# Performance work log

Hardware: AMD Instinct MI355X
Metric: run time of the kernel (lower is better)

Reference implementation:

```python
import jax, jax.numpy as jnp
import numpy as np

N_NODES = 100000
N_EDGES = 1600000
F_IN, H1, H2, N_CLS = 512, 180, 120, 40
NEG_SLOPE = 0.01  # F.leaky_relu default


def setup_inputs() -> dict:
    key = jax.random.key(0)
    ks = jax.random.split(key, 8)
    x = jax.random.normal(ks[0], (N_NODES, F_IN), dtype=jnp.float32)
    edge_index = jax.random.randint(ks[1], (2, N_EDGES), 0, N_NODES, dtype=jnp.int64)
    W1 = jax.random.normal(ks[2], (F_IN, H1), dtype=jnp.float32) / np.sqrt(F_IN)
    b1 = jnp.zeros((H1,), dtype=jnp.float32)
    W2 = jax.random.normal(ks[3], (H1, H2), dtype=jnp.float32) / np.sqrt(H1)
    b2 = jnp.zeros((H2,), dtype=jnp.float32)
    W3 = jax.random.normal(ks[4], (H2, N_CLS), dtype=jnp.float32) / np.sqrt(H2)
    b3 = jnp.zeros((N_CLS,), dtype=jnp.float32)
    return {"x": x, "edge_index": edge_index, "W1": W1, "b1": b1,
            "W2": W2, "b2": b2, "W3": W3, "b3": b3}


def _add_self_loops(edge_index, n):
    loop = jnp.arange(n, dtype=edge_index.dtype)
    src = jnp.concatenate([edge_index[0], loop])
    dst = jnp.concatenate([edge_index[1], loop])
    return src, dst


def _gcn_conv(h, src, dst, norm, W, b, n):
    # PyG GCNConv: linear transform first, then normalized scatter-add at dst.
    h = h @ W  # [N, out]
    msg = norm[:, None] * h[src]  # gather at source, per-edge scale
    out = jax.ops.segment_sum(msg, dst, num_segments=n)  # scatter-add at dest
    return out + b


def reference(x, edge_index, W1, b1, W2, b2, W3, b3):
    n = x.shape[0]
    src, dst = _add_self_loops(edge_index, n)
    # symmetric normalization deg^-1/2 * deg^-1/2 on self-loop-augmented graph
    ones = jnp.ones(dst.shape[0], dtype=x.dtype)
    deg = jax.ops.segment_sum(ones, dst, num_segments=n)
    dinv = jnp.where(deg > 0, jax.lax.rsqrt(deg), 0.0)
    norm = dinv[src] * dinv[dst]  # [E+N]

    h = _gcn_conv(x, src, dst, norm, W1, b1, n)
    h = jnp.where(h >= 0, h, NEG_SLOPE * h)
    h = _gcn_conv(h, src, dst, norm, W2, b2, n)
    h = jnp.where(h >= 0, h, NEG_SLOPE * h)
    logits = h @ W3 + b3
    return jax.nn.log_softmax(logits, axis=1)
```

## Files before the change

### kernel.cpp

```cpp
#include <hip/hip_runtime.h>
#include <math.h>

typedef __attribute__((ext_vector_type(8))) short short8;
typedef __attribute__((ext_vector_type(4))) float f32x4;

static constexpr int F_IN = 512;
static constexpr int H1V = 180, H1P = 192;
static constexpr int H2V = 120, H2P = 128;
static constexpr int NC  = 40,  NCP = 64;

__device__ inline unsigned f2bf(float f) {
    unsigned u = __float_as_uint(f);
    return (u + 0x7fffu + ((u >> 16) & 1u)) >> 16;
}
__device__ inline unsigned cvtpk(float lo, float hi) {
    unsigned r;
    asm("v_cvt_pk_bf16_f32 %0, %1, %2" : "=v"(r) : "v"(lo), "v"(hi));
    return r;
}
#define BLO(u) __uint_as_float((u) << 16)
#define BHI(u) __uint_as_float((u) & 0xffff0000u)

__device__ inline void gload_lds16(const void* gsrc, void* ldst) {
    __builtin_amdgcn_global_load_lds(
        (const __attribute__((address_space(1))) void*)gsrc,
        (__attribute__((address_space(3))) void*)ldst, 16, 0, 0);
}

__global__ void k_detect(const int* __restrict__ ei, int* __restrict__ flag) {
    int i = blockIdx.x * 256 + threadIdx.x;
    if (ei[2 * i + 1] != 0) flag[0] = 0;
}

__global__ void k_hist(const int* __restrict__ ei, int E, const int* __restrict__ flag,
                       int* __restrict__ deg, int* __restrict__ rank) {
    int e = blockIdx.x * 256 + threadIdx.x;
    if (e >= E) return;
    int d = flag[0] ? ei[2 * E + 2 * e] : ei[E + e];
    rank[e] = atomicAdd(&deg[d], 1);
}

__global__ void k_scan1(const int* __restrict__ deg, int* __restrict__ rp,
                        int* __restrict__ bsum, float* __restrict__ dinv, int n) {
    __shared__ int s[256];
    int t = threadIdx.x;
    int base = blockIdx.x * 1024 + t * 4;
    int v0 = (base + 0 < n) ? deg[base + 0] : 0;
    int v1 = (base + 1 < n) ? deg[base + 1] : 0;
    int v2 = (base + 2 < n) ? deg[base + 2] : 0;
    int v3 = (base + 3 < n) ? deg[base + 3] : 0;
    if (base + 0 < n) dinv[base + 0] = rsqrtf((float)(v0 + 1));
    if (base + 1 < n) dinv[base + 1] = rsqrtf((float)(v1 + 1));
    if (base + 2 < n) dinv[base + 2] = rsqrtf((float)(v2 + 1));
    if (base + 3 < n) dinv[base + 3] = rsqrtf((float)(v3 + 1));
    int sum = v0 + v1 + v2 + v3;
    s[t] = sum;
    __syncthreads();
    for (int off = 1; off < 256; off <<= 1) {
        int x = (t >= off) ? s[t - off] : 0;
        __syncthreads();
        s[t] += x;
        __syncthreads();
    }
    int run = s[t] - sum;
    if (t == 255) bsum[blockIdx.x] = s[255];
    if (base + 0 < n) rp[base + 0] = run; run += v0;
    if (base + 1 < n) rp[base + 1] = run; run += v1;
    if (base + 2 < n) rp[base + 2] = run; run += v2;
    if (base + 3 < n) rp[base + 3] = run;
}

__global__ void k_scan2(int* __restrict__ bsum, int nb) {
    __shared__ int s[128];
    int t = threadIdx.x;
    int v = (t < nb) ? bsum[t] : 0;
    s[t] = v;
    __syncthreads();
    for (int off = 1; off < 128; off <<= 1) {
        int x = (t >= off) ? s[t - off] : 0;
        __syncthreads();
        s[t] += x;
        __syncthreads();
    }
    if (t < nb) bsum[t] = s[t] - v;
}

__global__ void k_scan3(const int* __restrict__ bsum, int* __restrict__ rp,
                        int n, int E) {
    int i = blockIdx.x * 256 + threadIdx.x;
    if (i < n) {
        rp[i] = rp[i] + bsum[i >> 10];
    } else if (i == n) {
        rp[n] = E;
    }
}

__global__ __launch_bounds__(256) void k_fill(const int* __restrict__ ei, int E,
                                              const int* __restrict__ flag,
                                              const int* __restrict__ rp,
                                              const int* __restrict__ rank,
                                              int* __restrict__ csr,
                                              int bw, int chunk) {
    int bkt = blockIdx.x & 7;
    int lo = bkt * bw, hi = lo + bw;
    int ch = blockIdx.x >> 3;
    int e0 = ch * chunk;
    int e1 = min(E, e0 + chunk);
    bool i64 = flag[0] != 0;
    for (int e = e0 + (int)threadIdx.x; e < e1; e += 256) {
        int d = i64 ? ei[2 * E + 2 * e] : ei[E + e];
        if (d >= lo && d < hi) {
            int s = i64 ? ei[2 * e] : ei[e];
            csr[rp[d] + rank[e]] = s;
        }
    }
}

__global__ void k_prep(const float* __restrict__ W1, const float* __restrict__ W2,
                       const float* __restrict__ W3, const float* __restrict__ b1,
                       const float* __restrict__ b2, const float* __restrict__ b3,
                       unsigned short* __restrict__ W1s, unsigned short* __restrict__ W2s,
                       unsigned short* __restrict__ W3s, float* __restrict__ b1p,
                       float* __restrict__ b2p, float* __restrict__ b3p) {
    const int n1 = F_IN * H1P;
    const int n2 = n1 + H1P * H2P;
    const int n3 = n2 + H2P * NCP;
    const int n4 = n3 + H1P;
    const int n5 = n4 + H2P;
    const int n6 = n5 + NCP;
    int i = blockIdx.x * 256 + threadIdx.x;
    if (i < n1) {
        int k = i / H1P, c = i % H1P;
        float v = (c < H1V) ? W1[k * H1V + c] : 0.0f;
        W1s[(size_t)(k >> 3) * H1P * 8 + c * 8 + (k & 7)] = (unsigned short)f2bf(v);
    } else if (i < n2) {
        int j = i - n1;
        int k = j / H2P, c = j % H2P;
        float v = (k < H1V && c < H2V) ? W2[k * H2V + c] : 0.0f;
        W2s[(size_t)(k >> 3) * H2P * 8 + c * 8 + (k & 7)] = (unsigned short)f2bf(v);
    } else if (i < n3) {
        int j = i - n2;
        int k = j / NCP, c = j % NCP;
        float v = (k < H2V && c < NC) ? W3[k * NC + c] : 0.0f;
        W3s[(size_t)(k >> 3) * NCP * 8 + c * 8 + (k & 7)] = (unsigned short)f2bf(v);
    } else if (i < n4) {
        int c = i - n3;
        b1p[c] = (c < H1V) ? b1[c] : 0.0f;
    } else if (i < n5) {
        int c = i - n4;
        b2p[c] = (c < H2V) ? b2[c] : 0.0f;
    } else if (i < n6) {
        int c = i - n5;
        b3p[c] = (c < NC) ? b3[c] : -1e30f;
    }
}

__global__ __launch_bounds__(512) void k_gemm1(const float* __restrict__ X,
                                               const short8* __restrict__ Bs,
                                               const float* __restrict__ dinv,
                                               unsigned short* __restrict__ Hout,
                                               int M) {
    __shared__ float ldsf[8192];
    char* lds = (char*)ldsf;
    int t = threadIdx.x;
    int w = t >> 6, l = t & 63;
    int lr = l & 15, kg = l >> 4;
    int wr = w >> 2, wc = w & 3;
    int row0 = blockIdx.x * 128;
    int colb = wc * 48;

    f32x4 acc[4][3];
#pragma unroll
    for (int m = 0; m < 4; ++m)
#pragma unroll
        for (int nn = 0; nn < 3; ++nn) acc[m][nn] = (f32x4){0.f, 0.f, 0.f, 0.f};

    auto stage = [&](int kb, int buf) {
#pragma unroll
        for (int j = 0; j < 2; ++j) {
            int o = j * 8192 + t * 16;
            int row = o >> 7;
            int col4 = ((o >> 4) & 7) ^ (row & 7);
            int rowg = row0 + row;
            if (rowg >= M) rowg = M - 1;
            gload_lds16(X + (size_t)rowg * F_IN + kb + col4 * 4,
                        lds + buf * 16384 + j * 8192 + w * 1024);
        }
    };

    stage(0, 0);
    __syncthreads();

    for (int ts = 0; ts < 16; ++ts) {
        int cur = ts & 1;
        if (ts < 15) stage((ts + 1) * 32, cur ^ 1);
        short8 b[3];
#pragma unroll
        for (int nn = 0; nn < 3; ++nn)
            b[nn] = Bs[(size_t)(ts * 4 + kg) * H1P + colb + nn * 16 + lr];
        short8 a[4];
#pragma unroll
        for (int m = 0; m < 4; ++m) {
            int row = wr * 64 + m * 16 + lr;
            char* base = lds + cur * 16384 + row * 128;
            float4 v0 = *(const float4*)(base + (((2 * kg + 0) ^ (row & 7)) * 16));
            float4 v1 = *(const float4*)(base + (((2 * kg + 1) ^ (row & 7)) * 16));
            union { unsigned u[4]; short8 s; } cu;
            cu.u[0] = cvtpk(v0.x, v0.y);
            cu.u[1] = cvtpk(v0.z, v0.w);
            cu.u[2] = cvtpk(v1.x, v1.y);
            cu.u[3] = cvtpk(v1.z, v1.w);
            a[m] = cu.s;
        }
#pragma unroll
        for (int m = 0; m < 4; ++m)
#pragma unroll
            for (int nn = 0; nn < 3; ++nn)
                acc[m][nn] = __builtin_amdgcn_mfma_f32_16x16x32_bf16(a[m], b[nn], acc[m][nn], 0, 0, 0);
        __syncthreads();
    }

#pragma unroll
    for (int m = 0; m < 4; ++m) {
        int r4 = row0 + wr * 64 + m * 16 + kg * 4;
#pragma unroll
        for (int j = 0; j < 4; ++j) {
            int grow = r4 + j;
            if (grow < M) {
                float dv = dinv[grow];
#pragma unroll
                for (int nn = 0; nn < 3; ++nn)
                    Hout[(size_t)grow * H1P + colb + nn * 16 + lr] =
                        (unsigned short)f2bf(acc[m][nn][j] * dv);
            }
        }
    }
}

__global__ __launch_bounds__(512) void k_gemm2(const unsigned short* __restrict__ A,
                                               const short8* __restrict__ Bs,
                                               const float* __restrict__ dinv,
                                               unsigned short* __restrict__ Hout,
                                               int M) {
    __shared__ unsigned short ldsu[16384];
    char* lds = (char*)ldsu;
    int t = threadIdx.x;
    int w = t >> 6, l = t & 63;
    int lr = l & 15, kg = l >> 4;
    int wr = w >> 2, wc = w & 3;
    int row0 = blockIdx.x * 128;
    int colb = wc * 32;

    f32x4 acc[4][2];
#pragma unroll
    for (int m = 0; m < 4; ++m)
#pragma unroll
        for (int nn = 0; nn < 2; ++nn) acc[m][nn] = (f32x4){0.f, 0.f, 0.f, 0.f};

    auto stage = [&](int kb, int buf) {
#pragma unroll
        for (int j = 0; j < 2; ++j) {
            int o = j * 8192 + t * 16;
            int row = o >> 7;
            int chunk = ((o >> 4) & 7) ^ (row & 7);
            int rowg = row0 + row;
            if (rowg >= M) rowg = M - 1;
            gload_lds16(A + (size_t)rowg * H1P + kb + chunk * 8,
                        lds + buf * 16384 + j * 8192 + w * 1024);
        }
    };

    stage(0, 0);
    __syncthreads();

    for (int ts = 0; ts < 3; ++ts) {
        int cur = ts & 1;
        if (ts < 2) stage((ts + 1) * 64, cur ^ 1);
        short8 b[2][2];
#pragma unroll
        for (int kk = 0; kk < 2; ++kk)
#pragma unroll
            for (int nn = 0; nn < 2; ++nn)
                b[kk][nn] = Bs[(size_t)(ts * 8 + kk * 4 + kg) * H2P + colb + nn * 16 + lr];
        short8 a[2][4];
#pragma unroll
        for (int kk = 0; kk < 2; ++kk)
#pragma unroll
            for (int m = 0; m < 4; ++m) {
                int row = wr * 64 + m * 16 + lr;
                a[kk][m] = *(const short8*)(lds + cur * 16384 + row * 128 +
                                            (((kk * 4 + kg) ^ (row & 7)) * 16));
            }
#pragma unroll
        for (int kk = 0; kk < 2; ++kk)
#pragma unroll
            for (int m = 0; m < 4; ++m)
#pragma unroll
                for (int nn = 0; nn < 2; ++nn)
                    acc[m][nn] = __builtin_amdgcn_mfma_f32_16x16x32_bf16(a[kk][m], b[kk][nn], acc[m][nn], 0, 0, 0);
        __syncthreads();
    }

#pragma unroll
    for (int m = 0; m < 4; ++m) {
        int r4 = row0 + wr * 64 + m * 16 + kg * 4;
#pragma unroll
        for (int j = 0; j < 4; ++j) {
            int grow = r4 + j;
            if (grow < M) {
                float dv = dinv[grow];
#pragma unroll
                for (int nn = 0; nn < 2; ++nn)
                    Hout[(size_t)grow * H2P + colb + nn * 16 + lr] =
                        (unsigned short)f2bf(acc[m][nn][j] * dv);
            }
        }
    }
}

template <int CH, int OUTBF>
__global__ __launch_bounds__(256) void k_gat(const uint2* __restrict__ H,
                                             const float* __restrict__ dinv,
                                             const int* __restrict__ rp,
                                             const int* __restrict__ csr,
                                             const float* __restrict__ bias,
                                             void* __restrict__ outv, int n) {
    int wv = threadIdx.x >> 6, l = threadIdx.x & 63;
    int i = blockIdx.x * 4 + wv;
    if (i >= n) return;
    bool act = l < CH;
    int c = act ? l : 0;
    const uint2* Hr = H + c;

    float a0, a1, a2, a3;
    {
        uint2 v = Hr[(size_t)i * CH];
        a0 = BLO(v.x); a1 = BHI(v.x); a2 = BLO(v.y); a3 = BHI(v.y);
    }
    float p0 = 0.f, p1 = 0.f, p2 = 0.f, p3 = 0.f;

    int e0 = rp[i], e1 = rp[i + 1];
    int e = e0;
    for (; e + 7 < e1; e += 8) {
        int s[8];
#pragma unroll
        for (int q = 0; q < 8; ++q) s[q] = csr[e + q];
        uint2 v[8];
#pragma unroll
        for (int q = 0; q < 8; ++q) v[q] = Hr[(size_t)s[q] * CH];
#pragma unroll
        for (int q = 0; q < 8; q += 2) {
            a0 += BLO(v[q].x); a1 += BHI(v[q].x); a2 += BLO(v[q].y); a3 += BHI(v[q].y);
            p0 += BLO(v[q + 1].x); p1 += BHI(v[q + 1].x); p2 += BLO(v[q + 1].y); p3 += BHI(v[q + 1].y);
        }
    }
    for (; e + 3 < e1; e += 4) {
        int s0 = csr[e], s1 = csr[e + 1], s2 = csr[e + 2], s3 = csr[e + 3];
        uint2 va = Hr[(size_t)s0 * CH];
        uint2 vb = Hr[(size_t)s1 * CH];
        uint2 vc = Hr[(size_t)s2 * CH];
        uint2 vd = Hr[(size_t)s3 * CH];
        a0 += BLO(va.x); a1 += BHI(va.x); a2 += BLO(va.y); a3 += BHI(va.y);
        p0 += BLO(vb.x); p1 += BHI(vb.x); p2 += BLO(vb.y); p3 += BHI(vb.y);
        a0 += BLO(vc.x); a1 += BHI(vc.x); a2 += BLO(vc.y); a3 += BHI(vc.y);
        p0 += BLO(vd.x); p1 += BHI(vd.x); p2 += BLO(vd.y); p3 += BHI(vd.y);
    }
    for (; e < e1; ++e) {
        int s0 = csr[e];
        uint2 va = Hr[(size_t)s0 * CH];
        a0 += BLO(va.x); a1 += BHI(va.x); a2 += BLO(va.y); a3 += BHI(va.y);
    }
    a0 += p0; a1 += p1; a2 += p2; a3 += p3;

    float di = dinv[i];
    float4 bb = *(const float4*)(bias + 4 * c);
    float o0 = fmaf(di, a0, bb.x);
    float o1 = fmaf(di, a1, bb.y);
    float o2 = fmaf(di, a2, bb.z);
    float o3 = fmaf(di, a3, bb.w);
    o0 = o0 >= 0.f ? o0 : 0.01f * o0;
    o1 = o1 >= 0.f ? o1 : 0.01f * o1;
    o2 = o2 >= 0.f ? o2 : 0.01f * o2;
    o3 = o3 >= 0.f ? o3 : 0.01f * o3;
    if (act) {
        if (OUTBF) {
            uint2 r;
            r.x = (f2bf(o1) << 16) | f2bf(o0);
            r.y = (f2bf(o3) << 16) | f2bf(o2);
            ((uint2*)outv)[(size_t)i * CH + c] = r;
        } else {
            ((float4*)outv)[(size_t)i * CH + c] = make_float4(o0, o1, o2, o3);
        }
    }
}

__global__ __launch_bounds__(256) void k_gat2(const uint2* __restrict__ H,
                                              const float* __restrict__ dinv,
                                              const int* __restrict__ rp,
                                              const int* __restrict__ csr,
                                              const float* __restrict__ bias,
                                              uint2* __restrict__ out, int n) {
    int wv = threadIdx.x >> 6, l = threadIdx.x & 63;
    int half = l >> 5, c = l & 31;
    int i = blockIdx.x * 8 + wv * 2 + half;
    if (i >= n) return;
    const uint2* Hr = H + c;

    float a0, a1, a2, a3;
    {
        uint2 v = Hr[(size_t)i * 32];
        a0 = BLO(v.x); a1 = BHI(v.x); a2 = BLO(v.y); a3 = BHI(v.y);
    }
    float p0 = 0.f, p1 = 0.f, p2 = 0.f, p3 = 0.f;

    int e0 = rp[i], e1 = rp[i + 1];
    int e = e0;
    for (; e + 7 < e1; e += 8) {
        int s[8];
#pragma unroll
        for (int q = 0; q < 8; ++q) s[q] = csr[e + q];
        uint2 v[8];
#pragma unroll
        for (int q = 0; q < 8; ++q) v[q] = Hr[(size_t)s[q] * 32];
#pragma unroll
        for (int q = 0; q < 8; q += 2) {
            a0 += BLO(v[q].x); a1 += BHI(v[q].x); a2 += BLO(v[q].y); a3 += BHI(v[q].y);
            p0 += BLO(v[q + 1].x); p1 += BHI(v[q + 1].x); p2 += BLO(v[q + 1].y); p3 += BHI(v[q + 1].y);
        }
    }
    for (; e + 3 < e1; e += 4) {
        int s0 = csr[e], s1 = csr[e + 1], s2 = csr[e + 2], s3 = csr[e + 3];
        uint2 va = Hr[(size_t)s0 * 32];
        uint2 vb = Hr[(size_t)s1 * 32];
        uint2 vc = Hr[(size_t)s2 * 32];
        uint2 vd = Hr[(size_t)s3 * 32];
        a0 += BLO(va.x); a1 += BHI(va.x); a2 += BLO(va.y); a3 += BHI(va.y);
        p0 += BLO(vb.x); p1 += BHI(vb.x); p2 += BLO(vb.y); p3 += BHI(vb.y);
        a0 += BLO(vc.x); a1 += BHI(vc.x); a2 += BLO(vc.y); a3 += BHI(vc.y);
        p0 += BLO(vd.x); p1 += BHI(vd.x); p2 += BLO(vd.y); p3 += BHI(vd.y);
    }
    for (; e < e1; ++e) {
        int s0 = csr[e];
        uint2 va = Hr[(size_t)s0 * 32];
        a0 += BLO(va.x); a1 += BHI(va.x); a2 += BLO(va.y); a3 += BHI(va.y);
    }
    a0 += p0; a1 += p1; a2 += p2; a3 += p3;

    float di = dinv[i];
    float4 bb = *(const float4*)(bias + 4 * c);
    float o0 = fmaf(di, a0, bb.x);
    float o1 = fmaf(di, a1, bb.y);
    float o2 = fmaf(di, a2, bb.z);
    float o3 = fmaf(di, a3, bb.w);
    o0 = o0 >= 0.f ? o0 : 0.01f * o0;
    o1 = o1 >= 0.f ? o1 : 0.01f * o1;
    o2 = o2 >= 0.f ? o2 : 0.01f * o2;
    o3 = o3 >= 0.f ? o3 : 0.01f * o3;
    uint2 r;
    r.x = (f2bf(o1) << 16) | f2bf(o0);
    r.y = (f2bf(o3) << 16) | f2bf(o2);
    out[(size_t)i * 32 + c] = r;
}

__global__ __launch_bounds__(256) void k_out(const unsigned short* __restrict__ H,
                                             const short8* __restrict__ Bs,
                                             const float* __restrict__ b3p,
                                             float* __restrict__ out, int M) {
    int t = threadIdx.x;
    int w = t >> 6, l = t & 63;
    int lr = l & 15, kg = l >> 4;
    int row0 = blockIdx.x * 64 + w * 16;

    f32x4 acc[4];
#pragma unroll
    for (int f = 0; f < 4; ++f) acc[f] = (f32x4){0.f, 0.f, 0.f, 0.f};

    int rowa = row0 + lr;
    if (rowa >= M) rowa = M - 1;
    const unsigned short* arow = H + (size_t)rowa * H2P;

#pragma unroll
    for (int ks = 0; ks < 4; ++ks) {
        short8 a = *(const short8*)(arow + ks * 32 + kg * 8);
#pragma unroll
        for (int f = 0; f < 4; ++f) {
            short8 b = Bs[(size_t)(ks * 4 + kg) * NCP + f * 16 + lr];
            acc[f] = __builtin_amdgcn_mfma_f32_16x16x32_bf16(a, b, acc[f], 0, 0, 0);
        }
    }

    float bl[4];
#pragma unroll
    for (int f = 0; f < 4; ++f) bl[f] = b3p[f * 16 + lr];

#pragma unroll
    for (int j = 0; j < 4; ++j) {
        int grow = row0 + kg * 4 + j;
        float lg[4];
#pragma unroll
        for (int f = 0; f < 4; ++f) lg[f] = acc[f][j] + bl[f];
        float m = fmaxf(fmaxf(lg[0], lg[1]), fmaxf(lg[2], lg[3]));
#pragma unroll
        for (int d = 1; d < 16; d <<= 1) m = fmaxf(m, __shfl_xor(m, d));
        float s = expf(lg[0] - m) + expf(lg[1] - m) + expf(lg[2] - m) + expf(lg[3] - m);
#pragma unroll
        for (int d = 1; d < 16; d <<= 1) s += __shfl_xor(s, d);
        float lse = m + logf(s);
        if (grow < M) {
#pragma unroll
            for (int f = 0; f < 4; ++f) {
                int c = f * 16 + lr;
                if (c < NC) out[(size_t)grow * NC + c] = lg[f] - lse;
            }
        }
    }
}

extern "C" void kernel_launch(void* const* d_in, const int* in_sizes, int n_in,
                              void* d_out, int out_size, void* d_ws, size_t ws_size,
                              hipStream_t stream) {
    const float* x  = (const float*)d_in[0];
    const int*   ei = (const int*)d_in[1];
    const float* W1 = (const float*)d_in[2];
    const float* b1 = (const float*)d_in[3];
    const float* W2 = (const float*)d_in[4];
    const float* b2 = (const float*)d_in[5];
    const float* W3 = (const float*)d_in[6];
    const float* b3 = (const float*)d_in[7];
    float* outp = (float*)d_out;

    int n = in_sizes[0] / F_IN;
    int E = in_sizes[1] / 2;

    char* p = (char*)d_ws;
    auto alloc = [&](size_t bytes) -> char* {
        char* r = p;
        p += (bytes + 511) & ~(size_t)511;
        return r;
    };
    int*            flag   = (int*)alloc(4);
    int*            deg    = (int*)alloc((size_t)n * 4);
    float*          dinv   = (float*)alloc((size_t)n * 4);
    int*            rp     = (int*)alloc((size_t)(n + 1) * 4);
    int*            bsum   = (int*)alloc(4096);
    int*            rank   = (int*)alloc((size_t)E * 4);
    int*            csr    = (int*)alloc((size_t)E * 4);
    unsigned short* W1s    = (unsigned short*)alloc((size_t)F_IN * H1P * 2);
    unsigned short* W2s    = (unsigned short*)alloc((size_t)H1P * H2P * 2);
    unsigned short* W3s    = (unsigned short*)alloc((size_t)H2P * NCP * 2);
    float*          b1p    = (float*)alloc(H1P * 4);
    float*          b2p    = (float*)alloc(H2P * 4);
    float*          b3p    = (float*)alloc(NCP * 4);
    unsigned short* h1     = (unsigned short*)alloc((size_t)n * H1P * 2);
    unsigned short* h1agg  = (unsigned short*)alloc((size_t)n * H1P * 2);
    unsigned short* h2     = (unsigned short*)alloc((size_t)n * H2P * 2);
    unsigned short* h2agg  = (unsigned short*)alloc((size_t)n * H2P * 2);

    hipMemsetAsync(flag, 1, 4, stream);
    hipMemsetAsync(deg, 0, (size_t)n * 4, stream);

    k_detect<<<16, 256, 0, stream>>>(ei, flag);

    int eb = (E + 255) / 256;
    k_hist<<<eb, 256, 0, stream>>>(ei, E, flag, deg, rank);

    int nb = (n + 1023) / 1024;
    k_scan1<<<nb, 256, 0, stream>>>(deg, rp, bsum, dinv, n);
    k_scan2<<<1, 128, 0, stream>>>(bsum, nb);
    k_scan3<<<(n + 1 + 255) / 256, 256, 0, stream>>>(bsum, rp, n, E);

    int bw = (n + 7) / 8;
    int nch = 256;
    int chunk = (E + nch - 1) / nch;
    k_fill<<<nch * 8, 256, 0, stream>>>(ei, E, flag, rp, rank, csr, bw, chunk);

    k_prep<<<514, 256, 0, stream>>>(W1, W2, W3, b1, b2, b3, W1s, W2s, W3s, b1p, b2p, b3p);

    int gb = (n + 127) / 128;
    k_gemm1<<<gb, 512, 0, stream>>>(x, (const short8*)W1s, dinv, h1, n);
    k_gat<H1P / 4, 1><<<(n + 3) / 4, 256, 0, stream>>>((const uint2*)h1, dinv, rp, csr, b1p, h1agg, n);
    k_gemm2<<<gb, 512, 0, stream>>>(h1agg, (const short8*)W2s, dinv, h2, n);
    k_gat2<<<(n + 7) / 8, 256, 0, stream>>>((const uint2*)h2, dinv, rp, csr, b2p, (uint2*)h2agg, n);
    k_out<<<(n + 63) / 64, 256, 0, stream>>>(h2agg, (const short8*)W3s, b3p, outp, n);
}
```

Baseline: 377.6 us.

## Quantize layer-1 features to int8 with per-row scales for aggregation

The first GEMM now emits int8 features with a per-row scale, computed by a cross-wave row-max reduction through LDS, instead of bf16. A new gather kernel dequantizes while accumulating neighbours, so each per-edge gather reads 4 bytes per lane instead of 8, halving the traffic of the first aggregation. Separately, weight prep and index-width detection are merged into one init kernel and the flag and degree memsets into one, removing a launch and a memset. The int8 step adds quantization error on top of bf16 and an extra scale load per edge.

```diff
diff --git a/kernel.cpp b/kernel.cpp
--- a/kernel.cpp
+++ b/kernel.cpp
@@ -27,108 +27,25 @@
         (__attribute__((address_space(3))) void*)ldst, 16, 0, 0);
 }
 
-__global__ void k_detect(const int* __restrict__ ei, int* __restrict__ flag) {
-    int i = blockIdx.x * 256 + threadIdx.x;
-    if (ei[2 * i + 1] != 0) flag[0] = 0;
-}
-
-__global__ void k_hist(const int* __restrict__ ei, int E, const int* __restrict__ flag,
-                       int* __restrict__ deg, int* __restrict__ rank) {
-    int e = blockIdx.x * 256 + threadIdx.x;
-    if (e >= E) return;
-    int d = flag[0] ? ei[2 * E + 2 * e] : ei[E + e];
-    rank[e] = atomicAdd(&deg[d], 1);
-}
-
-__global__ void k_scan1(const int* __restrict__ deg, int* __restrict__ rp,
-                        int* __restrict__ bsum, float* __restrict__ dinv, int n) {
-    __shared__ int s[256];
-    int t = threadIdx.x;
-    int base = blockIdx.x * 1024 + t * 4;
-    int v0 = (base + 0 < n) ? deg[base + 0] : 0;
-    int v1 = (base + 1 < n) ? deg[base + 1] : 0;
-    int v2 = (base + 2 < n) ? deg[base + 2] : 0;
-    int v3 = (base + 3 < n) ? deg[base + 3] : 0;
-    if (base + 0 < n) dinv[base + 0] = rsqrtf((float)(v0 + 1));
-    if (base + 1 < n) dinv[base + 1] = rsqrtf((float)(v1 + 1));
-    if (base + 2 < n) dinv[base + 2] = rsqrtf((float)(v2 + 1));
-    if (base + 3 < n) dinv[base + 3] = rsqrtf((float)(v3 + 1));
-    int sum = v0 + v1 + v2 + v3;
-    s[t] = sum;
-    __syncthreads();
-    for (int off = 1; off < 256; off <<= 1) {
-        int x = (t >= off) ? s[t - off] : 0;
-        __syncthreads();
-        s[t] += x;
-        __syncthreads();
-    }
-    int run = s[t] - sum;
-    if (t == 255) bsum[blockIdx.x] = s[255];
-    if (base + 0 < n) rp[base + 0] = run; run += v0;
-    if (base + 1 < n) rp[base + 1] = run; run += v1;
-    if (base + 2 < n) rp[base + 2] = run; run += v2;
-    if (base + 3 < n) rp[base + 3] = run;
-}
-
-__global__ void k_scan2(int* __restrict__ bsum, int nb) {
-    __shared__ int s[128];
-    int t = threadIdx.x;
-    int v = (t < nb) ? bsum[t] : 0;
-    s[t] = v;
-    __syncthreads();
-    for (int off = 1; off < 128; off <<= 1) {
-        int x = (t >= off) ? s[t - off] : 0;
-        __syncthreads();
-        s[t] += x;
-        __syncthreads();
-    }
-    if (t < nb) bsum[t] = s[t] - v;
-}
-
-__global__ void k_scan3(const int* __restrict__ bsum, int* __restrict__ rp,
-                        int n, int E) {
-    int i = blockIdx.x * 256 + threadIdx.x;
-    if (i < n) {
-        rp[i] = rp[i] + bsum[i >> 10];
-    } else if (i == n) {
-        rp[n] = E;
-    }
-}
-
-__global__ __launch_bounds__(256) void k_fill(const int* __restrict__ ei, int E,
-                                              const int* __restrict__ flag,
-                                              const int* __restrict__ rp,
-                                              const int* __restrict__ rank,
-                                              int* __restrict__ csr,
-                                              int bw, int chunk) {
-    int bkt = blockIdx.x & 7;
-    int lo = bkt * bw, hi = lo + bw;
-    int ch = blockIdx.x >> 3;
-    int e0 = ch * chunk;
-    int e1 = min(E, e0 + chunk);
-    bool i64 = flag[0] != 0;
-    for (int e = e0 + (int)threadIdx.x; e < e1; e += 256) {
-        int d = i64 ? ei[2 * E + 2 * e] : ei[E + e];
-        if (d >= lo && d < hi) {
-            int s = i64 ? ei[2 * e] : ei[e];
-            csr[rp[d] + rank[e]] = s;
-        }
-    }
-}
-
-__global__ void k_prep(const float* __restrict__ W1, const float* __restrict__ W2,
+__global__ void k_init(const int* __restrict__ ei, int* __restrict__ flag,
+                       const float* __restrict__ W1, const float* __restrict__ W2,
                        const float* __restrict__ W3, const float* __restrict__ b1,
                        const float* __restrict__ b2, const float* __restrict__ b3,
                        unsigned short* __restrict__ W1s, unsigned short* __restrict__ W2s,
                        unsigned short* __restrict__ W3s, float* __restrict__ b1p,
                        float* __restrict__ b2p, float* __restrict__ b3p) {
+    if (blockIdx.x < 16) {
+        int i = blockIdx.x * 256 + threadIdx.x;
+        if (ei[2 * i + 1] != 0) flag[0] = 1;
+        return;
+    }
     const int n1 = F_IN * H1P;
     const int n2 = n1 + H1P * H2P;
     const int n3 = n2 + H2P * NCP;
     const int n4 = n3 + H1P;
     const int n5 = n4 + H2P;
     const int n6 = n5 + NCP;
-    int i = blockIdx.x * 256 + threadIdx.x;
+    int i = (blockIdx.x - 16) * 256 + threadIdx.x;
     if (i < n1) {
         int k = i / H1P, c = i % H1P;
         float v = (c < H1V) ? W1[k * H1V + c] : 0.0f;
@@ -155,10 +72,96 @@
     }
 }
 
+__global__ void k_hist(const int* __restrict__ ei, int E, const int* __restrict__ flag,
+                       int* __restrict__ deg, int* __restrict__ rank) {
+    int e = blockIdx.x * 256 + threadIdx.x;
+    if (e >= E) return;
+    bool i64 = (flag[0] == 0);
+    int d = i64 ? ei[2 * E + 2 * e] : ei[E + e];
+    rank[e] = atomicAdd(&deg[d], 1);
+}
+
+__global__ void k_scan1(const int* __restrict__ deg, int* __restrict__ rp,
+                        int* __restrict__ bsum, float* __restrict__ dinv, int n) {
+    __shared__ int s[256];
+    int t = threadIdx.x;
+    int base = blockIdx.x * 1024 + t * 4;
+    int v0 = (base + 0 < n) ? deg[base + 0] : 0;
+    int v1 = (base + 1 < n) ? deg[base + 1] : 0;
+    int v2 = (base + 2 < n) ? deg[base + 2] : 0;
+    int v3 = (base + 3 < n) ? deg[base + 3] : 0;
+    if (base + 0 < n) dinv[base + 0] = rsqrtf((float)(v0 + 1));
+    if (base + 1 < n) dinv[base + 1] = rsqrtf((float)(v1 + 1));
+    if (base + 2 < n) dinv[base + 2] = rsqrtf((float)(v2 + 1));
+    if (base + 3 < n) dinv[base + 3] = rsqrtf((float)(v3 + 1));
+    int sum = v0 + v1 + v2 + v3;
+    s[t] = sum;
+    __syncthreads();
+    for (int off = 1; off < 256; off <<= 1) {
+        int x = (t >= off) ? s[t - off] : 0;
+        __syncthreads();
+        s[t] += x;
+        __syncthreads();
+    }
+    int run = s[t] - sum;
+    if (t == 255) bsum[blockIdx.x] = s[255];
+    if (base + 0 < n) rp[base + 0] = run; run += v0;
+    if (base + 1 < n) rp[base + 1] = run; run += v1;
+    if (base + 2 < n) rp[base + 2] = run; run += v2;
+    if (base + 3 < n) rp[base + 3] = run;
+}
+
+__global__ void k_scan2(int* __restrict__ bsum, int nb) {
+    __shared__ int s[128];
+    int t = threadIdx.x;
+    int v = (t < nb) ? bsum[t] : 0;
+    s[t] = v;
+    __syncthreads();
+    for (int off = 1; off < 128; off <<= 1) {
+        int x = (t >= off) ? s[t - off] : 0;
+        __syncthreads();
+        s[t] += x;
+        __syncthreads();
+    }
+    if (t < nb) bsum[t] = s[t] - v;
+}
+
+__global__ void k_scan3(const int* __restrict__ bsum, int* __restrict__ rp,
+                        int n, int E) {
+    int i = blockIdx.x * 256 + threadIdx.x;
+    if (i < n) {
+        rp[i] = rp[i] + bsum[i >> 10];
+    } else if (i == n) {
+        rp[n] = E;
+    }
+}
+
+__global__ __launch_bounds__(256) void k_fill(const int* __restrict__ ei, int E,
+                                              const int* __restrict__ flag,
+                                              const int* __restrict__ rp,
+                                              const int* __restrict__ rank,
+                                              int* __restrict__ csr,
+                                              int bw, int chunk) {
+    int bkt = blockIdx.x & 7;
+    int lo = bkt * bw, hi = lo + bw;
+    int ch = blockIdx.x >> 3;
+    int e0 = ch * chunk;
+    int e1 = min(E, e0 + chunk);
+    bool i64 = (flag[0] == 0);
+    for (int e = e0 + (int)threadIdx.x; e < e1; e += 256) {
+        int d = i64 ? ei[2 * E + 2 * e] : ei[E + e];
+        if (d >= lo && d < hi) {
+            int s = i64 ? ei[2 * e] : ei[e];
+            csr[rp[d] + rank[e]] = s;
+        }
+    }
+}
+
 __global__ __launch_bounds__(512) void k_gemm1(const float* __restrict__ X,
                                                const short8* __restrict__ Bs,
                                                const float* __restrict__ dinv,
-                                               unsigned short* __restrict__ Hout,
+                                               signed char* __restrict__ Hq,
+                                               float* __restrict__ sc,
                                                int M) {
     __shared__ float ldsf[8192];
     char* lds = (char*)ldsf;
@@ -220,20 +223,122 @@
         __syncthreads();
     }
 
+    float* rmaxp = (float*)lds;
 #pragma unroll
     for (int m = 0; m < 4; ++m) {
-        int r4 = row0 + wr * 64 + m * 16 + kg * 4;
 #pragma unroll
         for (int j = 0; j < 4; ++j) {
-            int grow = r4 + j;
-            if (grow < M) {
-                float dv = dinv[grow];
-#pragma unroll
-                for (int nn = 0; nn < 3; ++nn)
-                    Hout[(size_t)grow * H1P + colb + nn * 16 + lr] =
-                        (unsigned short)f2bf(acc[m][nn][j] * dv);
+            int rl = wr * 64 + m * 16 + kg * 4 + j;
+            int grow = row0 + rl;
+            float dv = (grow < M) ? dinv[grow] : 0.f;
+            float lm = 0.f;
+#pragma unroll
+            for (int nn = 0; nn < 3; ++nn)
+                lm = fmaxf(lm, fabsf(acc[m][nn][j] * dv));
+#pragma unroll
+            for (int d = 1; d < 16; d <<= 1)
+                lm = fmaxf(lm, __shfl_xor(lm, d));
+            if (lr == 0) rmaxp[rl * 4 + wc] = lm;
+        }
+    }
+    __syncthreads();
+#pragma unroll
+    for (int m = 0; m < 4; ++m) {
+#pragma unroll
+        for (int j = 0; j < 4; ++j) {
+            int rl = wr * 64 + m * 16 + kg * 4 + j;
+            int grow = row0 + rl;
+            if (grow >= M) continue;
+            float dv = dinv[grow];
+            float rm = fmaxf(fmaxf(rmaxp[rl * 4 + 0], rmaxp[rl * 4 + 1]),
+                             fmaxf(rmaxp[rl * 4 + 2], rmaxp[rl * 4 + 3]));
+            float inv = (rm > 0.f) ? 127.0f / rm : 0.f;
+            if (wc == 0 && lr == 0) sc[grow] = rm * (1.0f / 127.0f);
+#pragma unroll
+            for (int nn = 0; nn < 3; ++nn) {
+                float v = acc[m][nn][j] * dv * inv;
+                v = fminf(fmaxf(rintf(v), -127.f), 127.f);
+                Hq[(size_t)grow * H1P + colb + nn * 16 + lr] = (signed char)(int)v;
             }
         }
+    }
+}
+
+__global__ __launch_bounds__(256) void k_gat1q(const signed char* __restrict__ Hq,
+                                               const float* __restrict__ sc,
+                                               const float* __restrict__ dinv,
+                                               const int* __restrict__ rp,
+                                               const int* __restrict__ csr,
+                                               const float* __restrict__ bias,
+                                               uint2* __restrict__ out, int n) {
+    int wv = threadIdx.x >> 6, l = threadIdx.x & 63;
+    int i = blockIdx.x * 4 + wv;
+    if (i >= n) return;
+    bool act = l < 48;
+    int c = act ? l : 0;
+    const unsigned* Hr = (const unsigned*)(Hq + c * 4);
+
+    float a0, a1, a2, a3;
+    {
+        unsigned w0 = Hr[(size_t)i * 48];
+        float s0 = sc[i];
+        a0 = (float)(signed char)(w0) * s0;
+        a1 = (float)(signed char)(w0 >> 8) * s0;
+        a2 = (float)(signed char)(w0 >> 16) * s0;
+        a3 = (float)(signed char)(w0 >> 24) * s0;
+    }
+    float p0 = 0.f, p1 = 0.f, p2 = 0.f, p3 = 0.f;
+
+    int e0 = rp[i], e1 = rp[i + 1];
+    int e = e0;
+    for (; e + 7 < e1; e += 8) {
+        int s[8];
+#pragma unroll
+        for (int q = 0; q < 8; ++q) s[q] = csr[e + q];
+        float scs[8];
+#pragma unroll
+        for (int q = 0; q < 8; ++q) scs[q] = sc[s[q]];
+        unsigned v[8];
+#pragma unroll
+        for (int q = 0; q < 8; ++q) v[q] = Hr[(size_t)s[q] * 48];
+#pragma unroll
+        for (int q = 0; q < 8; q += 2) {
+            a0 = fmaf((float)(signed char)(v[q]), scs[q], a0);
+            a1 = fmaf((float)(signed char)(v[q] >> 8), scs[q], a1);
+            a2 = fmaf((float)(signed char)(v[q] >> 16), scs[q], a2);
+            a3 = fmaf((float)(signed char)(v[q] >> 24), scs[q], a3);
+            p0 = fmaf((float)(signed char)(v[q + 1]), scs[q + 1], p0);
+            p1 = fmaf((float)(signed char)(v[q + 1] >> 8), scs[q + 1], p1);
+            p2 = fmaf((float)(signed char)(v[q + 1] >> 16), scs[q + 1], p2);
+            p3 = fmaf((float)(signed char)(v[q + 1] >> 24), scs[q + 1], p3);
+        }
+    }
+    for (; e < e1; ++e) {
+        int s0 = csr[e];
+        float sq = sc[s0];
+        unsigned w0 = Hr[(size_t)s0 * 48];
+        a0 = fmaf((float)(signed char)(w0), sq, a0);
+        a1 = fmaf((float)(signed char)(w0 >> 8), sq, a1);
+        a2 = fmaf((float)(signed char)(w0 >> 16), sq, a2);
+        a3 = fmaf((float)(signed char)(w0 >> 24), sq, a3);
+    }
+    a0 += p0; a1 += p1; a2 += p2; a3 += p3;
+
+    float di = dinv[i];
+    float4 bb = *(const float4*)(bias + 4 * c);
+    float o0 = fmaf(di, a0, bb.x);
+    float o1 = fmaf(di, a1, bb.y);
+    float o2 = fmaf(di, a2, bb.z);
+    float o3 = fmaf(di, a3, bb.w);
+    o0 = o0 >= 0.f ? o0 : 0.01f * o0;
+    o1 = o1 >= 0.f ? o1 : 0.01f * o1;
+    o2 = o2 >= 0.f ? o2 : 0.01f * o2;
+    o3 = o3 >= 0.f ? o3 : 0.01f * o3;
+    if (act) {
+        uint2 r;
+        r.x = (f2bf(o1) << 16) | f2bf(o0);
+        r.y = (f2bf(o3) << 16) | f2bf(o2);
+        out[(size_t)i * 48 + c] = r;
     }
 }
 
@@ -314,82 +419,6 @@
                     Hout[(size_t)grow * H2P + colb + nn * 16 + lr] =
                         (unsigned short)f2bf(acc[m][nn][j] * dv);
             }
-        }
-    }
-}
-
-template <int CH, int OUTBF>
-__global__ __launch_bounds__(256) void k_gat(const uint2* __restrict__ H,
-                                             const float* __restrict__ dinv,
-                                             const int* __restrict__ rp,
-                                             const int* __restrict__ csr,
-                                             const float* __restrict__ bias,
-                                             void* __restrict__ outv, int n) {
-    int wv = threadIdx.x >> 6, l = threadIdx.x & 63;
-    int i = blockIdx.x * 4 + wv;
-    if (i >= n) return;
-    bool act = l < CH;
-    int c = act ? l : 0;
-    const uint2* Hr = H + c;
-
-    float a0, a1, a2, a3;
-    {
-        uint2 v = Hr[(size_t)i * CH];
-        a0 = BLO(v.x); a1 = BHI(v.x); a2 = BLO(v.y); a3 = BHI(v.y);
-    }
-    float p0 = 0.f, p1 = 0.f, p2 = 0.f, p3 = 0.f;
-
-    int e0 = rp[i], e1 = rp[i + 1];
-    int e = e0;
-    for (; e + 7 < e1; e += 8) {
-        int s[8];
-#pragma unroll
-        for (int q = 0; q < 8; ++q) s[q] = csr[e + q];
-        uint2 v[8];
-#pragma unroll
-        for (int q = 0; q < 8; ++q) v[q] = Hr[(size_t)s[q] * CH];
-#pragma unroll
-        for (int q = 0; q < 8; q += 2) {
-            a0 += BLO(v[q].x); a1 += BHI(v[q].x); a2 += BLO(v[q].y); a3 += BHI(v[q].y);
-            p0 += BLO(v[q + 1].x); p1 += BHI(v[q + 1].x); p2 += BLO(v[q + 1].y); p3 += BHI(v[q + 1].y);
-        }
-    }
-    for (; e + 3 < e1; e += 4) {
-        int s0 = csr[e], s1 = csr[e + 1], s2 = csr[e + 2], s3 = csr[e + 3];
-        uint2 va = Hr[(size_t)s0 * CH];
-        uint2 vb = Hr[(size_t)s1 * CH];
-        uint2 vc = Hr[(size_t)s2 * CH];
-        uint2 vd = Hr[(size_t)s3 * CH];
-        a0 += BLO(va.x); a1 += BHI(va.x); a2 += BLO(va.y); a3 += BHI(va.y);
-        p0 += BLO(vb.x); p1 += BHI(vb.x); p2 += BLO(vb.y); p3 += BHI(vb.y);
-        a0 += BLO(vc.x); a1 += BHI(vc.x); a2 += BLO(vc.y); a3 += BHI(vc.y);
-        p0 += BLO(vd.x); p1 += BHI(vd.x); p2 += BLO(vd.y); p3 += BHI(vd.y);
-    }
-    for (; e < e1; ++e) {
-        int s0 = csr[e];
-        uint2 va = Hr[(size_t)s0 * CH];
-        a0 += BLO(va.x); a1 += BHI(va.x); a2 += BLO(va.y); a3 += BHI(va.y);
-    }
-    a0 += p0; a1 += p1; a2 += p2; a3 += p3;
-
-    float di = dinv[i];
-    float4 bb = *(const float4*)(bias + 4 * c);
-    float o0 = fmaf(di, a0, bb.x);
-    float o1 = fmaf(di, a1, bb.y);
-    float o2 = fmaf(di, a2, bb.z);
-    float o3 = fmaf(di, a3, bb.w);
-    o0 = o0 >= 0.f ? o0 : 0.01f * o0;
-    o1 = o1 >= 0.f ? o1 : 0.01f * o1;
-    o2 = o2 >= 0.f ? o2 : 0.01f * o2;
-    o3 = o3 >= 0.f ? o3 : 0.01f * o3;
-    if (act) {
-        if (OUTBF) {
-            uint2 r;
-            r.x = (f2bf(o1) << 16) | f2bf(o0);
-            r.y = (f2bf(o3) << 16) | f2bf(o2);
-            ((uint2*)outv)[(size_t)i * CH + c] = r;
-        } else {
-            ((float4*)outv)[(size_t)i * CH + c] = make_float4(o0, o1, o2, o3);
         }
     }
 }
@@ -538,8 +567,9 @@
         p += (bytes + 511) & ~(size_t)511;
         return r;
     };
-    int*            flag   = (int*)alloc(4);
-    int*            deg    = (int*)alloc((size_t)n * 4);
+    int*            fd     = (int*)alloc((size_t)(n + 1) * 4);
+    int*            flag   = fd;
+    int*            deg    = fd + 1;
     float*          dinv   = (float*)alloc((size_t)n * 4);
     int*            rp     = (int*)alloc((size_t)(n + 1) * 4);
     int*            bsum   = (int*)alloc(4096);
@@ -551,15 +581,16 @@
     float*          b1p    = (float*)alloc(H1P * 4);
     float*          b2p    = (float*)alloc(H2P * 4);
     float*          b3p    = (float*)alloc(NCP * 4);
-    unsigned short* h1     = (unsigned short*)alloc((size_t)n * H1P * 2);
+    signed char*    h1q    = (signed char*)alloc((size_t)n * H1P);
+    float*          sc     = (float*)alloc((size_t)n * 4);
     unsigned short* h1agg  = (unsigned short*)alloc((size_t)n * H1P * 2);
     unsigned short* h2     = (unsigned short*)alloc((size_t)n * H2P * 2);
     unsigned short* h2agg  = (unsigned short*)alloc((size_t)n * H2P * 2);
 
-    hipMemsetAsync(flag, 1, 4, stream);
-    hipMemsetAsync(deg, 0, (size_t)n * 4, stream);
-
-    k_detect<<<16, 256, 0, stream>>>(ei, flag);
+    hipMemsetAsync(fd, 0, (size_t)(n + 1) * 4, stream);
+
+    k_init<<<530, 256, 0, stream>>>(ei, flag, W1, W2, W3, b1, b2, b3,
+                                    W1s, W2s, W3s, b1p, b2p, b3p);
 
     int eb = (E + 255) / 256;
     k_hist<<<eb, 256, 0, stream>>>(ei, E, flag, deg, rank);
@@ -574,12 +605,12 @@
     int chunk = (E + nch - 1) / nch;
     k_fill<<<nch * 8, 256, 0, stream>>>(ei, E, flag, rp, rank, csr, bw, chunk);
 
-    k_prep<<<514, 256, 0, stream>>>(W1, W2, W3, b1, b2, b3, W1s, W2s, W3s, b1p, b2p, b3p);
-
     int gb = (n + 127) / 128;
-    k_gemm1<<<gb, 512, 0, stream>>>(x, (const short8*)W1s, dinv, h1, n);
-    k_gat<H1P / 4, 1><<<(n + 3) / 4, 256, 0, stream>>>((const uint2*)h1, dinv, rp, csr, b1p, h1agg, n);
+    k_gemm1<<<gb, 512, 0, stream>>>(x, (const short8*)W1s, dinv, h1q, sc, n);
+    k_gat1q<<<(n + 3) / 4, 256, 0, stream>>>(h1q, sc, dinv, rp, csr, b1p,
+                                             (uint2*)h1agg, n);
     k_gemm2<<<gb, 512, 0, stream>>>(h1agg, (const short8*)W2s, dinv, h2, n);
-    k_gat2<<<(n + 7) / 8, 256, 0, stream>>>((const uint2*)h2, dinv, rp, csr, b2p, (uint2*)h2agg, n);
+    k_gat2<<<(n + 7) / 8, 256, 0, stream>>>((const uint2*)h2, dinv, rp, csr, b2p,
+                                            (uint2*)h2agg, n);
     k_out<<<(n + 63) / 64, 256, 0, stream>>>(h2agg, (const short8*)W3s, b3p, outp, n);
 }
```

Result: no change. 373.1 us (-1.2%).
